# Kernel tuning notes

Measured on AMD Instinct MI355X. Metric: run time of the kernel, lower is better.

## Reference

```python
import jax, jax.numpy as jnp
import numpy as np

TEMPERATURE = 0.1
NUM_CLASSES = 4  # matches fill_max of labels
NEG_INF = -1e9
EPS = 1e-6


def setup_inputs() -> dict:
    key = jax.random.key(0)
    k1, k2 = jax.random.split(key)
    emb = jax.random.normal(k1, (2, 128, 64, 64), dtype=jnp.float32)
    labels = jax.random.randint(k2, (2, 64, 64), 0, NUM_CLASSES, dtype=jnp.int32)
    return {"emb": emb, "labels": labels}


def reference(emb, labels):
    B, C, H, W = emb.shape
    e = emb.transpose(0, 2, 3, 1).reshape(B * H * W, C)      # [N, C]
    lab = labels.reshape(B * H * W)                           # [N]
    # F.normalize(dim=1) with eps clamp
    norm = jnp.maximum(jnp.linalg.norm(e, axis=1, keepdims=True), 1e-12)
    e = e / norm
    n = e.shape[0]
    logits = (e @ e.T) / TEMPERATURE                          # [N, N]
    diag = jnp.arange(n)
    logits = logits.at[diag, diag].set(NEG_INF)               # mask self
    ex = jnp.exp(logits)                                      # [N, N]
    same = lab[:, None] == lab[None, :]                       # [N, N] bool
    pos_sum = jnp.sum(jnp.where(same, ex, 0.0), axis=1)       # [N]
    tot_sum = jnp.sum(ex, axis=1)                             # [N]
    row_loss = -jnp.log(pos_sum / (tot_sum + EPS))            # [N]
    # per-class mean, averaged over classes present (== torch.unique loop)
    sums = jax.ops.segment_sum(row_loss, lab, num_segments=NUM_CLASSES)
    counts = jax.ops.segment_sum(jnp.ones_like(row_loss), lab, num_segments=NUM_CLASSES)
    present = counts > 0
    per_cls = jnp.where(present, sums / jnp.maximum(counts, 1.0), 0.0)
    return per_cls.sum() / present.sum()
```

## Files before the change

kernel.cpp:

```cpp
#include <hip/hip_runtime.h>
#include <hip/hip_bf16.h>

#define N_PIX 8192
#define C_DIM 128
#define HW 4096
#define PRESCALE 3.7982825f
#define NUM_CLASSES 4

typedef __attribute__((ext_vector_type(8))) short short8;
typedef __attribute__((ext_vector_type(4))) float float4v;


__global__ __launch_bounds__(256) void normscale_kernel(const float* __restrict__ emb,
                                                        unsigned short* __restrict__ ebfT,
                                                        float* __restrict__ pz) {
    const int tid = threadIdx.x;
    const int p16 = tid & 15;
    const int g = tid >> 4;
    const int n = blockIdx.x * 16 + p16;
    const int b = n >> 12;
    const int hw = n & (HW - 1);
    const float* base = emb + b * (C_DIM * HW) + hw;

    float v[8];
    float ss = 0.f;
#pragma unroll
    for (int i = 0; i < 8; ++i) {
        v[i] = base[(g * 8 + i) * HW];
        ss += v[i] * v[i];
    }
    ss += __shfl_xor(ss, 16, 64);
    ss += __shfl_xor(ss, 32, 64);
    __shared__ float red[4][16];
    const int wv = tid >> 6;
    if ((tid & 63) < 16) red[wv][p16] = ss;
    __syncthreads();
    float tot = red[0][p16] + red[1][p16] + red[2][p16] + red[3][p16];
    float inv = PRESCALE / fmaxf(sqrtf(tot), 1e-12f);

    unsigned short us[8];
#pragma unroll
    for (int i = 0; i < 8; ++i) {
        __hip_bfloat16 h = __float2bfloat16(v[i] * inv);
        us[i] = *reinterpret_cast<unsigned short*>(&h);
    }
    const int s = g >> 2, quad = g & 3;
    unsigned short* dst = ebfT + (((blockIdx.x * 4 + s) * 64 + quad * 16 + p16) << 3);
    *reinterpret_cast<short8*>(dst) = *reinterpret_cast<short8*>(us);

    if (blockIdx.x < 64) pz[blockIdx.x * 256 + tid] = 0.f;
}

__global__ __launch_bounds__(256, 4) void pairwise_kernel(const unsigned short* __restrict__ ebfT,
                                                          const int* __restrict__ lab,
                                                          float* __restrict__ pos,
                                                          float* __restrict__ tot) {
    const int wave = threadIdx.x >> 6;
    const int lane = threadIdx.x & 63;
    const int quad = lane >> 4;
    const int lq = lane & 15;

    const int I0 = blockIdx.x * 128 + wave * 32;
    const int Jbase = blockIdx.y * 256;

    short8 afrag[2][4];
#pragma unroll
    for (int a = 0; a < 2; ++a) {
        const unsigned short* ab = ebfT + ((((I0 >> 4) + a) * 4) * 64 + lane) * 8;
#pragma unroll
        for (int s = 0; s < 4; ++s)
            afrag[a][s] = *reinterpret_cast<const short8*>(ab + s * 512);
    }
    int lab_row[2][4];
#pragma unroll
    for (int a = 0; a < 2; ++a)
#pragma unroll
        for (int r = 0; r < 4; ++r) lab_row[a][r] = lab[I0 + a * 16 + quad * 4 + r];

    float tacc[2][4] = {};
    float pacc[2][4] = {};

#define EPILOGUE(A, ACC, MASKED)                                            \
    {                                                                       \
        _Pragma("unroll") for (int r = 0; r < 4; ++r) {                     \
            float ex = __builtin_amdgcn_exp2f(ACC[r]);                      \
            if (MASKED) ex = (lq == quad * 4 + r) ? 0.f : ex;               \
            tacc[A][r] += ex;                                               \
            pacc[A][r] += (lab_row[A][r] == lab_col) ? ex : 0.f;            \
        }                                                                   \
    }

    const unsigned short* bbase = ebfT + ((Jbase >> 4) * 4 * 64 + lane) * 8;

    for (int t = 0; t < 16; ++t) {
        const int J = Jbase + t * 16;
        const int lab_col = lab[J + lq];
        const unsigned short* bt = bbase + t * 2048;
        short8 bfrag[4];
#pragma unroll
        for (int s = 0; s < 4; ++s)
            bfrag[s] = *reinterpret_cast<const short8*>(bt + s * 512);

        float4v acc0 = {0.f, 0.f, 0.f, 0.f};
        float4v acc1 = {0.f, 0.f, 0.f, 0.f};
#pragma unroll
        for (int s = 0; s < 4; ++s) {
            acc0 = __builtin_amdgcn_mfma_f32_16x16x32_bf16(afrag[0][s], bfrag[s], acc0, 0, 0, 0);
            acc1 = __builtin_amdgcn_mfma_f32_16x16x32_bf16(afrag[1][s], bfrag[s], acc1, 0, 0, 0);
        }
        if (J == I0) EPILOGUE(0, acc0, true) else EPILOGUE(0, acc0, false);
        if (J == I0 + 16) EPILOGUE(1, acc1, true) else EPILOGUE(1, acc1, false);
    }
#undef EPILOGUE

#pragma unroll
    for (int a = 0; a < 2; ++a) {
#pragma unroll
        for (int r = 0; r < 4; ++r) {
            float t = tacc[a][r], p = pacc[a][r];
#pragma unroll
            for (int off = 1; off < 16; off <<= 1) {
                t += __shfl_xor(t, off, 64);
                p += __shfl_xor(p, off, 64);
            }
            if (lq == 0) {
                const int row = I0 + a * 16 + quad * 4 + r;
                atomicAdd(&tot[row], t);
                atomicAdd(&pos[row], p);
            }
        }
    }
}

__global__ __launch_bounds__(1024) void finalize_kernel(const float* __restrict__ pos,
                                                        const float* __restrict__ tot,
                                                        const int* __restrict__ lab,
                                                        float* __restrict__ out) {
    const int tid = threadIdx.x;
    float ls[NUM_CLASSES] = {0.f, 0.f, 0.f, 0.f};
    float lc[NUM_CLASSES] = {0.f, 0.f, 0.f, 0.f};
#pragma unroll
    for (int it = 0; it < N_PIX / 1024; ++it) {
        const int n = it * 1024 + tid;
        float rl = logf(tot[n] + 1e-6f) - logf(pos[n]);
        int c = lab[n];
#pragma unroll
        for (int k = 0; k < NUM_CLASSES; ++k) {
            if (c == k) {
                ls[k] += rl;
                lc[k] += 1.f;
            }
        }
    }
#pragma unroll
    for (int off = 1; off < 64; off <<= 1) {
#pragma unroll
        for (int k = 0; k < NUM_CLASSES; ++k) {
            ls[k] += __shfl_xor(ls[k], off, 64);
            lc[k] += __shfl_xor(lc[k], off, 64);
        }
    }
    __shared__ float ssum[16][NUM_CLASSES];
    __shared__ float scnt[16][NUM_CLASSES];
    const int wid = tid >> 6;
    if ((tid & 63) == 0) {
#pragma unroll
        for (int k = 0; k < NUM_CLASSES; ++k) {
            ssum[wid][k] = ls[k];
            scnt[wid][k] = lc[k];
        }
    }
    __syncthreads();
    if (tid == 0) {
        float acc = 0.f;
        int present = 0;
        for (int k = 0; k < NUM_CLASSES; ++k) {
            float s = 0.f, c = 0.f;
            for (int w = 0; w < 16; ++w) {
                s += ssum[w][k];
                c += scnt[w][k];
            }
            if (c > 0.f) {
                acc += s / c;
                present++;
            }
        }
        out[0] = acc / (float)(present > 0 ? present : 1);
    }
}

extern "C" void kernel_launch(void* const* d_in, const int* in_sizes, int n_in,
                              void* d_out, int out_size, void* d_ws, size_t ws_size,
                              hipStream_t stream) {
    const float* emb = (const float*)d_in[0];
    const int* lab = (const int*)d_in[1];
    float* out = (float*)d_out;

    unsigned short* ebfT = (unsigned short*)d_ws;
    float* pos = (float*)((char*)d_ws + N_PIX * C_DIM * 2);
    float* tot = pos + N_PIX;

    normscale_kernel<<<N_PIX / 16, 256, 0, stream>>>(emb, ebfT, pos);

    dim3 grid(N_PIX / 128, 32);
    pairwise_kernel<<<grid, 256, 0, stream>>>(ebfT, lab, pos, tot);

    finalize_kernel<<<1, 1024, 0, stream>>>(pos, tot, lab, out);
}
```

Measured before the change: 97.22 us.

## Exploit symmetry of similarity matrix to compute only upper-triangular tiles

Uses the symmetry of the Gram matrix: each off-diagonal 128x128 tile is computed once and its exp values are added both to the row sums and, through shared-memory column accumulators, to the column sums of the mirrored rows. The grid becomes 64x33 panel pairs with a cyclic diagonal offset, roughly halving MFMA and exp work. In exchange it adds a per-tile cross-quad shuffle, shared-memory atomics, extra global atomics for the column panel, and block barriers.

New measurement: 118.1 us. +21.4%, slower.

```diff
diff --git a/kernel.cpp b/kernel.cpp
--- a/kernel.cpp
+++ b/kernel.cpp
@@ -55,13 +55,28 @@
                                                           const int* __restrict__ lab,
                                                           float* __restrict__ pos,
                                                           float* __restrict__ tot) {
+    const int bi = blockIdx.x;
+    const int d = blockIdx.y;
+    if (d == 32 && bi >= 32) return;
+    const int jp = (bi + d) & 63;
+    const int Ipanel = bi << 7;
+    const int Jpanel = jp << 7;
+    const bool offdiag = (d != 0);
+
+    __shared__ float colT[128];
+    __shared__ float colP[128];
+
     const int wave = threadIdx.x >> 6;
     const int lane = threadIdx.x & 63;
     const int quad = lane >> 4;
     const int lq = lane & 15;
 
-    const int I0 = blockIdx.x * 128 + wave * 32;
-    const int Jbase = blockIdx.y * 256;
+    if (threadIdx.x < 128) {
+        colT[threadIdx.x] = 0.f;
+        colP[threadIdx.x] = 0.f;
+    }
+
+    const int I0 = Ipanel + wave * 32;
 
     short8 afrag[2][4];
 #pragma unroll
@@ -80,20 +95,24 @@
     float tacc[2][4] = {};
     float pacc[2][4] = {};
 
-#define EPILOGUE(A, ACC, MASKED)                                            \
+    if (offdiag) __syncthreads();
+
+#define EPILOGUE(A, ACC, MASKED, OFFD)                                      \
     {                                                                       \
         _Pragma("unroll") for (int r = 0; r < 4; ++r) {                     \
             float ex = __builtin_amdgcn_exp2f(ACC[r]);                      \
             if (MASKED) ex = (lq == quad * 4 + r) ? 0.f : ex;               \
             tacc[A][r] += ex;                                               \
-            pacc[A][r] += (lab_row[A][r] == lab_col) ? ex : 0.f;            \
+            float pxe = (lab_row[A][r] == lab_col) ? ex : 0.f;              \
+            pacc[A][r] += pxe;                                              \
+            if (OFFD) { colTs += ex; colPs += pxe; }                        \
         }                                                                   \
     }
 
-    const unsigned short* bbase = ebfT + ((Jbase >> 4) * 4 * 64 + lane) * 8;
-
-    for (int t = 0; t < 16; ++t) {
-        const int J = Jbase + t * 16;
+    const unsigned short* bbase = ebfT + ((Jpanel >> 4) * 4 * 64 + lane) * 8;
+
+    for (int t = 0; t < 8; ++t) {
+        const int J = Jpanel + t * 16;
         const int lab_col = lab[J + lq];
         const unsigned short* bt = bbase + t * 2048;
         short8 bfrag[4];
@@ -108,8 +127,25 @@
             acc0 = __builtin_amdgcn_mfma_f32_16x16x32_bf16(afrag[0][s], bfrag[s], acc0, 0, 0, 0);
             acc1 = __builtin_amdgcn_mfma_f32_16x16x32_bf16(afrag[1][s], bfrag[s], acc1, 0, 0, 0);
         }
-        if (J == I0) EPILOGUE(0, acc0, true) else EPILOGUE(0, acc0, false);
-        if (J == I0 + 16) EPILOGUE(1, acc1, true) else EPILOGUE(1, acc1, false);
+
+        float colTs = 0.f, colPs = 0.f;
+        if (offdiag) {
+            EPILOGUE(0, acc0, false, true)
+            EPILOGUE(1, acc1, false, true)
+            colTs += __shfl_xor(colTs, 16, 64);
+            colTs += __shfl_xor(colTs, 32, 64);
+            colPs += __shfl_xor(colPs, 16, 64);
+            colPs += __shfl_xor(colPs, 32, 64);
+            if (quad == 0) {
+                atomicAdd(&colT[t * 16 + lq], colTs);
+                atomicAdd(&colP[t * 16 + lq], colPs);
+            }
+        } else {
+            const bool m0 = (J == I0);
+            const bool m1 = (J == I0 + 16);
+            if (m0) EPILOGUE(0, acc0, true, false) else EPILOGUE(0, acc0, false, false);
+            if (m1) EPILOGUE(1, acc1, true, false) else EPILOGUE(1, acc1, false, false);
+        }
     }
 #undef EPILOGUE
 
@@ -128,6 +164,14 @@
                 atomicAdd(&tot[row], t);
                 atomicAdd(&pos[row], p);
             }
+        }
+    }
+
+    if (offdiag) {
+        __syncthreads();
+        if (threadIdx.x < 128) {
+            atomicAdd(&tot[Jpanel + threadIdx.x], colT[threadIdx.x]);
+            atomicAdd(&pos[Jpanel + threadIdx.x], colP[threadIdx.x]);
         }
     }
 }
@@ -202,7 +246,7 @@
 
     normscale_kernel<<<N_PIX / 16, 256, 0, stream>>>(emb, ebfT, pos);
 
-    dim3 grid(N_PIX / 128, 32);
+    dim3 grid(64, 33);
     pairwise_kernel<<<grid, 256, 0, stream>>>(ebfT, lab, pos, tot);
 
     finalize_kernel<<<1, 1024, 0, stream>>>(pos, tot, lab, out);
```

## Exploit Gram matrix symmetry to compute only upper-triangular panel pairs

Applied to the files above, without the earlier changes.

The pairwise kernel now maps each block to a panel pair (bi, bi+d). Because e·eᵀ is symmetric, each off-diagonal 128x128 tile is computed once. Its row sums go to the I rows as before, and its column sums are reduced across quads and atomically added to the J rows. Diagonal panels are processed separately with self-masking, once per row panel. This roughly halves MFMA and exp work. In exchange it adds many more global atomics, with contention among the four waves on the same column addresses, and makes load balance across blocks uneven.

New measurement: 95.26 us. -2.0%, faster.

```diff
diff --git a/kernel.cpp b/kernel.cpp
--- a/kernel.cpp
+++ b/kernel.cpp
@@ -55,13 +55,19 @@
                                                           const int* __restrict__ lab,
                                                           float* __restrict__ pos,
                                                           float* __restrict__ tot) {
+    const int bi = blockIdx.x;
+    const int d = blockIdx.y + 1;
+    if (d == 32 && bi >= 32) return;
+    const int jp = (bi + d) & 63;
+    const int Ipanel = bi << 7;
+    const int Jpanel = jp << 7;
+
     const int wave = threadIdx.x >> 6;
     const int lane = threadIdx.x & 63;
     const int quad = lane >> 4;
     const int lq = lane & 15;
 
-    const int I0 = blockIdx.x * 128 + wave * 32;
-    const int Jbase = blockIdx.y * 256;
+    const int I0 = Ipanel + wave * 32;
 
     short8 afrag[2][4];
 #pragma unroll
@@ -79,6 +85,54 @@
 
     float tacc[2][4] = {};
     float pacc[2][4] = {};
+
+    {
+        const unsigned short* bbase = ebfT + ((Jpanel >> 4) * 4 * 64 + lane) * 8;
+        for (int t = 0; t < 8; ++t) {
+            const int lab_col = lab[Jpanel + t * 16 + lq];
+            const unsigned short* bt = bbase + t * 2048;
+            short8 bfrag[4];
+#pragma unroll
+            for (int s = 0; s < 4; ++s)
+                bfrag[s] = *reinterpret_cast<const short8*>(bt + s * 512);
+
+            float4v acc0 = {0.f, 0.f, 0.f, 0.f};
+            float4v acc1 = {0.f, 0.f, 0.f, 0.f};
+#pragma unroll
+            for (int s = 0; s < 4; ++s) {
+                acc0 = __builtin_amdgcn_mfma_f32_16x16x32_bf16(afrag[0][s], bfrag[s], acc0, 0, 0, 0);
+                acc1 = __builtin_amdgcn_mfma_f32_16x16x32_bf16(afrag[1][s], bfrag[s], acc1, 0, 0, 0);
+            }
+
+            float colTs = 0.f, colPs = 0.f;
+#pragma unroll
+            for (int r = 0; r < 4; ++r) {
+                float ex = __builtin_amdgcn_exp2f(acc0[r]);
+                tacc[0][r] += ex;
+                float pxe = (lab_row[0][r] == lab_col) ? ex : 0.f;
+                pacc[0][r] += pxe;
+                colTs += ex;
+                colPs += pxe;
+            }
+#pragma unroll
+            for (int r = 0; r < 4; ++r) {
+                float ex = __builtin_amdgcn_exp2f(acc1[r]);
+                tacc[1][r] += ex;
+                float pxe = (lab_row[1][r] == lab_col) ? ex : 0.f;
+                pacc[1][r] += pxe;
+                colTs += ex;
+                colPs += pxe;
+            }
+            colTs += __shfl_xor(colTs, 16, 64);
+            colTs += __shfl_xor(colTs, 32, 64);
+            colPs += __shfl_xor(colPs, 16, 64);
+            colPs += __shfl_xor(colPs, 32, 64);
+            if (quad == 0) {
+                atomicAdd(&tot[Jpanel + t * 16 + lq], colTs);
+                atomicAdd(&pos[Jpanel + t * 16 + lq], colPs);
+            }
+        }
+    }
 
 #define EPILOGUE(A, ACC, MASKED)                                            \
     {                                                                       \
@@ -89,27 +143,27 @@
             pacc[A][r] += (lab_row[A][r] == lab_col) ? ex : 0.f;            \
         }                                                                   \
     }
-
-    const unsigned short* bbase = ebfT + ((Jbase >> 4) * 4 * 64 + lane) * 8;
-
-    for (int t = 0; t < 16; ++t) {
-        const int J = Jbase + t * 16;
-        const int lab_col = lab[J + lq];
-        const unsigned short* bt = bbase + t * 2048;
-        short8 bfrag[4];
-#pragma unroll
-        for (int s = 0; s < 4; ++s)
-            bfrag[s] = *reinterpret_cast<const short8*>(bt + s * 512);
-
-        float4v acc0 = {0.f, 0.f, 0.f, 0.f};
-        float4v acc1 = {0.f, 0.f, 0.f, 0.f};
-#pragma unroll
-        for (int s = 0; s < 4; ++s) {
-            acc0 = __builtin_amdgcn_mfma_f32_16x16x32_bf16(afrag[0][s], bfrag[s], acc0, 0, 0, 0);
-            acc1 = __builtin_amdgcn_mfma_f32_16x16x32_bf16(afrag[1][s], bfrag[s], acc1, 0, 0, 0);
-        }
-        if (J == I0) EPILOGUE(0, acc0, true) else EPILOGUE(0, acc0, false);
-        if (J == I0 + 16) EPILOGUE(1, acc1, true) else EPILOGUE(1, acc1, false);
+    if (d == 1) {
+        const unsigned short* bbase = ebfT + ((Ipanel >> 4) * 4 * 64 + lane) * 8;
+        for (int t = 0; t < 8; ++t) {
+            const int J = Ipanel + t * 16;
+            const int lab_col = lab[J + lq];
+            const unsigned short* bt = bbase + t * 2048;
+            short8 bfrag[4];
+#pragma unroll
+            for (int s = 0; s < 4; ++s)
+                bfrag[s] = *reinterpret_cast<const short8*>(bt + s * 512);
+
+            float4v acc0 = {0.f, 0.f, 0.f, 0.f};
+            float4v acc1 = {0.f, 0.f, 0.f, 0.f};
+#pragma unroll
+            for (int s = 0; s < 4; ++s) {
+                acc0 = __builtin_amdgcn_mfma_f32_16x16x32_bf16(afrag[0][s], bfrag[s], acc0, 0, 0, 0);
+                acc1 = __builtin_amdgcn_mfma_f32_16x16x32_bf16(afrag[1][s], bfrag[s], acc1, 0, 0, 0);
+            }
+            if (J == I0) EPILOGUE(0, acc0, true) else EPILOGUE(0, acc0, false);
+            if (J == I0 + 16) EPILOGUE(1, acc1, true) else EPILOGUE(1, acc1, false);
+        }
     }
 #undef EPILOGUE
 
@@ -202,7 +256,7 @@
 
     normscale_kernel<<<N_PIX / 16, 256, 0, stream>>>(emb, ebfT, pos);
 
-    dim3 grid(N_PIX / 128, 32);
+    dim3 grid(64, 32);
     pairwise_kernel<<<grid, 256, 0, stream>>>(ebfT, lab, pos, tot);
 
     finalize_kernel<<<1, 1024, 0, stream>>>(pos, tot, lab, out);
```
